# Kernel tuning notes

Hardware: AMD Instinct MI355X
Metric: run time of the kernel (lower is better)

Reference implementation:

```python
import jax, jax.numpy as jnp
import numpy as np

B, S, D, VOCAB = 64, 2048, 256, 288

def setup_inputs() -> dict:
    key = jax.random.key(0)
    k1, k2, k3 = jax.random.split(key, 3)
    TE = jax.random.randint(k1, (B, S, 2), 0, VOCAB, dtype=jnp.int64)
    W1 = jax.random.normal(k2, (VOCAB + 7, D), dtype=jnp.float32) * 0.05
    b1 = jnp.zeros((D,), dtype=jnp.float32)
    W2 = jax.random.normal(k3, (D, D), dtype=jnp.float32) * 0.05
    b2 = jnp.zeros((D,), dtype=jnp.float32)
    return {"TE": TE, "T": VOCAB, "W1": W1, "b1": b1, "W2": W2, "b2": b2}

def reference(TE, T, W1, b1, W2, b2):
    # one_hot(day,7)||one_hot(time,T) @ W1  ==  gather rows of W1 and add
    day = TE[..., 0].astype(jnp.int32) % 7          # [B, S]
    tod = TE[..., 1].astype(jnp.int32) % T          # [B, S]
    h = W1[day] + W1[7 + tod] + b1                  # [B, S, D]  (Linear 1)
    h = jax.nn.relu(h)
    out = jnp.einsum('bsd,de->bse', h, W2) + b2     # [B, S, D]  (Linear 2)
    return out[:, :, None, :]                       # [B, S, 1, D]
```

## Files before the change

kernel.cpp:

```cpp
#include <hip/hip_runtime.h>
#include <hip/hip_bf16.h>


typedef __bf16 bf16x4 __attribute__((ext_vector_type(4)));
typedef __bf16 bf16x8 __attribute__((ext_vector_type(8)));
typedef float  f32x4  __attribute__((ext_vector_type(4)));

#define M_TOTAL   131072
#define BM        128


__global__ __launch_bounds__(64) void prep_all(const float* __restrict__ W1,
                                               const float* __restrict__ b1,
                                               const float* __restrict__ W2,
                                               __bf16* __restrict__ W2S,
                                               __bf16* __restrict__ Htab,
                                               const int* __restrict__ TE32,
                                               int* __restrict__ flag, int T) {
    const int b = blockIdx.x, lane = threadIdx.x;
    const int nTab = 7 * T;
    if (b < nTab) {
        const float* __restrict__ wa = W1 + (b / T) * 256;
        const float* __restrict__ wb = W1 + (7 + b % T) * 256;
        f32x4 a = *(const f32x4*)(wa + lane * 4);
        f32x4 c = *(const f32x4*)(wb + lane * 4);
        f32x4 d = *(const f32x4*)(b1 + lane * 4);
        bf16x4 h;
#pragma unroll
        for (int j = 0; j < 4; ++j) h[j] = (__bf16)fmaxf(a[j] + c[j] + d[j], 0.0f);
        *(bf16x4*)(Htab + b * 256 + lane * 4) = h;
    } else {
        const int wb = b - nTab;
#pragma unroll
        for (int q = 0; q < 2; ++q) {
            int c = (wb * 64 + lane) * 2 + q;
            int l = c & 63, ksnt = c >> 6;
            int ks = ksnt & 7, nt = ksnt >> 3;
            int n  = nt * 16 + (l & 15);
            int k0 = ks * 32 + (l >> 4) * 8;
            bf16x8 w;
#pragma unroll
            for (int j = 0; j < 8; ++j) w[j] = (__bf16)W2[(k0 + j) * 256 + n];
            *(bf16x8*)(W2S + c * 8) = w;
        }
        if (wb == 0) {
            int v = 0;
            for (int i = lane; i < 2048; i += 64) v |= TE32[2 * i + 1];
            unsigned long long nz = __ballot(v != 0);
            if (lane == 0) *flag = (nz == 0ull) ? 1 : 0;
        }
    }
}

__global__ __launch_bounds__(256, 3) void temb_gemm(
        const int*   __restrict__ TE32,
        const __bf16* __restrict__ Htab,
        const __bf16* __restrict__ W2S,
        const float* __restrict__ b2,
        const int*   __restrict__ flag,
        float* __restrict__ out, int T)
{
    __shared__ __bf16 Bs[4 * 8 * 512];

    const int is64 = *flag;
    const int tid  = threadIdx.x;
    const int wave = tid >> 6;
    const int lane = tid & 63;
    const int m    = lane & 15;
    const int quad = lane >> 4;
    const int rowBase = blockIdx.x * BM + wave * 32;

    int code[2];
#pragma unroll
    for (int t = 0; t < 2; ++t) {
        const int row = rowBase + t * 16 + m;
        int day, tod;
        if (is64) { int4 te = *(const int4*)(TE32 + 4 * row); day = te.x; tod = te.z; }
        else      { int2 te = *(const int2*)(TE32 + 2 * row); day = te.x; tod = te.y; }
        code[t] = (day % 7) * T + (tod % T);
    }
    bf16x8 hfrag[2][8];
#pragma unroll
    for (int t = 0; t < 2; ++t)
#pragma unroll
        for (int ks = 0; ks < 8; ++ks)
            hfrag[t][ks] = *(const bf16x8*)(Htab + code[t] * 256 + ks * 32 + quad * 8);

    const bf16x8* __restrict__ gsrc = (const bf16x8*)W2S + tid;
    bf16x8* __restrict__ ldst = (bf16x8*)Bs + tid;
    const bf16x8* __restrict__ lsrc = (const bf16x8*)Bs;

    bf16x8 stage[8];
#pragma unroll
    for (int q = 0; q < 8; ++q) stage[q] = gsrc[q * 256];

    for (int g = 0; g < 4; ++g) {
#pragma unroll
        for (int q = 0; q < 8; ++q) ldst[q * 256] = stage[q];
        __syncthreads();
        if (g < 3) {
#pragma unroll
            for (int q = 0; q < 8; ++q) stage[q] = gsrc[(g + 1) * 2048 + q * 256];
        }
#pragma unroll
        for (int ntl = 0; ntl < 4; ++ntl) {
            const int nt = g * 4 + ntl;
            f32x4 acc0 = {0.f, 0.f, 0.f, 0.f};
            f32x4 acc1 = {0.f, 0.f, 0.f, 0.f};
#pragma unroll
            for (int ks = 0; ks < 8; ++ks) {
                bf16x8 wfrag = lsrc[(ntl * 8 + ks) * 64 + lane];
                acc0 = __builtin_amdgcn_mfma_f32_16x16x32_bf16(wfrag, hfrag[0][ks], acc0, 0, 0, 0);
                acc1 = __builtin_amdgcn_mfma_f32_16x16x32_bf16(wfrag, hfrag[1][ks], acc1, 0, 0, 0);
            }
            const f32x4 bias = *(const f32x4*)(b2 + nt * 16 + quad * 4);
            f32x4 v0, v1;
#pragma unroll
            for (int r = 0; r < 4; ++r) { v0[r] = acc0[r] + bias[r]; v1[r] = acc1[r] + bias[r]; }
            float* p0 = out + (rowBase + m) * 256 + nt * 16 + quad * 4;
            *(f32x4*)p0 = v0;
            *(f32x4*)(p0 + 16 * 256) = v1;
        }
        __syncthreads();
    }
}

extern "C" void kernel_launch(void* const* d_in, const int* in_sizes, int n_in,
                              void* d_out, int out_size, void* d_ws, size_t ws_size,
                              hipStream_t stream) {
    const int*   TE = (const int*)  d_in[0];
    const float* W1 = (const float*)d_in[2];
    const float* b1 = (const float*)d_in[3];
    const float* W2 = (const float*)d_in[4];
    const float* b2 = (const float*)d_in[5];
    const int T = in_sizes[2] / 256 - 7;

    __bf16* W2S  = (__bf16*)d_ws;
    __bf16* Htab = (__bf16*)((char*)d_ws + 131072);
    int*    flag = (int*)((char*)d_ws + 131072 + (size_t)7 * T * 512);
    float*  out  = (float*)d_out;

    prep_all<<<7 * T + 64, 64, 0, stream>>>(W1, b1, W2, W2S, Htab, TE, flag, T);
    temb_gemm<<<M_TOTAL / BM, 256, 0, stream>>>(TE, Htab, W2S, b2, flag, out, T);
}
```

Measured before the change: 166.4 us.

## Precompute full output table per (day,tod) code and gather rows

Because the output depends only on the pair (day, tod), the change computes the full 7*T x 256 output table once with a small MFMA GEMM. The main kernel then becomes a pure gather that copies table rows to the output by code. This removes the per-row GEMM over all 131072 rows and leaves a memory-bound copy bounded by the output write. It needs extra workspace and falls back to the old path if the workspace is too small. It also fixes negative-modulo handling.

```diff
diff --git a/kernel.cpp b/kernel.cpp
--- a/kernel.cpp
+++ b/kernel.cpp
@@ -52,6 +52,108 @@
     }
 }
 
+__global__ __launch_bounds__(256, 3) void otab_gemm(
+        const __bf16* __restrict__ Htab,
+        const __bf16* __restrict__ W2S,
+        const float* __restrict__ b2,
+        float* __restrict__ Otab, int T)
+{
+    __shared__ __bf16 Bs[4 * 8 * 512];
+
+    const int tid  = threadIdx.x;
+    const int wave = tid >> 6;
+    const int lane = tid & 63;
+    const int m    = lane & 15;
+    const int quad = lane >> 4;
+    const int rowBase = blockIdx.x * BM + wave * 32;
+    const int nTab = 7 * T;
+
+    int code[2];
+#pragma unroll
+    for (int t = 0; t < 2; ++t) {
+        int row = rowBase + t * 16 + m;
+        code[t] = row < nTab ? row : nTab - 1;
+    }
+    bf16x8 hfrag[2][8];
+#pragma unroll
+    for (int t = 0; t < 2; ++t)
+#pragma unroll
+        for (int ks = 0; ks < 8; ++ks)
+            hfrag[t][ks] = *(const bf16x8*)(Htab + code[t] * 256 + ks * 32 + quad * 8);
+
+    const bf16x8* __restrict__ gsrc = (const bf16x8*)W2S + tid;
+    bf16x8* __restrict__ ldst = (bf16x8*)Bs + tid;
+    const bf16x8* __restrict__ lsrc = (const bf16x8*)Bs;
+
+    bf16x8 stage[8];
+#pragma unroll
+    for (int q = 0; q < 8; ++q) stage[q] = gsrc[q * 256];
+
+    for (int g = 0; g < 4; ++g) {
+#pragma unroll
+        for (int q = 0; q < 8; ++q) ldst[q * 256] = stage[q];
+        __syncthreads();
+        if (g < 3) {
+#pragma unroll
+            for (int q = 0; q < 8; ++q) stage[q] = gsrc[(g + 1) * 2048 + q * 256];
+        }
+#pragma unroll
+        for (int ntl = 0; ntl < 4; ++ntl) {
+            const int nt = g * 4 + ntl;
+            f32x4 acc0 = {0.f, 0.f, 0.f, 0.f};
+            f32x4 acc1 = {0.f, 0.f, 0.f, 0.f};
+#pragma unroll
+            for (int ks = 0; ks < 8; ++ks) {
+                bf16x8 wfrag = lsrc[(ntl * 8 + ks) * 64 + lane];
+                acc0 = __builtin_amdgcn_mfma_f32_16x16x32_bf16(wfrag, hfrag[0][ks], acc0, 0, 0, 0);
+                acc1 = __builtin_amdgcn_mfma_f32_16x16x32_bf16(wfrag, hfrag[1][ks], acc1, 0, 0, 0);
+            }
+            const f32x4 bias = *(const f32x4*)(b2 + nt * 16 + quad * 4);
+            f32x4 v0, v1;
+#pragma unroll
+            for (int r = 0; r < 4; ++r) { v0[r] = acc0[r] + bias[r]; v1[r] = acc1[r] + bias[r]; }
+            float* p0 = Otab + (rowBase + m) * 256 + nt * 16 + quad * 4;
+            *(f32x4*)p0 = v0;
+            *(f32x4*)(p0 + 16 * 256) = v1;
+        }
+        __syncthreads();
+    }
+}
+
+__global__ __launch_bounds__(256) void gather_out(
+        const int*   __restrict__ TE32,
+        const float* __restrict__ Otab,
+        const int*   __restrict__ flag,
+        float* __restrict__ out, int T)
+{
+    __shared__ int codes[64];
+    const int tid  = threadIdx.x;
+    const int wave = tid >> 6;
+    const int lane = tid & 63;
+    const int rowBase = blockIdx.x * 64;
+
+    if (tid < 64) {
+        const int is64 = *flag;
+        const int row = rowBase + tid;
+        int d32, t32;
+        if (is64) { int4 te = *(const int4*)(TE32 + 4 * row); d32 = te.x; t32 = te.z; }
+        else      { int2 te = *(const int2*)(TE32 + 2 * row); d32 = te.x; t32 = te.y; }
+        int day = d32 % 7; if (day < 0) day += 7;
+        int tod = t32 % T; if (tod < 0) tod += T;
+        codes[tid] = day * T + tod;
+    }
+    __syncthreads();
+
+    const float* src0 = Otab + lane * 4;
+    float*       dst0 = out + (size_t)rowBase * 256 + (size_t)wave * 16 * 256 + lane * 4;
+#pragma unroll
+    for (int r = 0; r < 16; ++r) {
+        const int c = codes[wave * 16 + r];
+        f32x4 v = *(const f32x4*)(src0 + (size_t)c * 256);
+        *(f32x4*)(dst0 + (size_t)r * 256) = v;
+    }
+}
+
 __global__ __launch_bounds__(256, 3) void temb_gemm(
         const int*   __restrict__ TE32,
         const __bf16* __restrict__ Htab,
@@ -77,7 +179,9 @@
         int day, tod;
         if (is64) { int4 te = *(const int4*)(TE32 + 4 * row); day = te.x; tod = te.z; }
         else      { int2 te = *(const int2*)(TE32 + 2 * row); day = te.x; tod = te.y; }
-        code[t] = (day % 7) * T + (tod % T);
+        int dm = day % 7; if (dm < 0) dm += 7;
+        int tm = tod % T; if (tm < 0) tm += T;
+        code[t] = dm * T + tm;
     }
     bf16x8 hfrag[2][8];
 #pragma unroll
@@ -135,11 +239,25 @@
     const float* b2 = (const float*)d_in[5];
     const int T = in_sizes[2] / 256 - 7;
 
+    const int otab_blocks = (7 * T + BM - 1) / BM;
+    const int otab_rows   = otab_blocks * BM;
+
+    const size_t hoff = 131072;
+    const size_t foff = hoff + (size_t)7 * T * 512;
+    const size_t ooff = foff + 256;
+    const size_t need = ooff + (size_t)otab_rows * 1024;
+
     __bf16* W2S  = (__bf16*)d_ws;
-    __bf16* Htab = (__bf16*)((char*)d_ws + 131072);
-    int*    flag = (int*)((char*)d_ws + 131072 + (size_t)7 * T * 512);
+    __bf16* Htab = (__bf16*)((char*)d_ws + hoff);
+    int*    flag = (int*)  ((char*)d_ws + foff);
+    float*  Otab = (float*)((char*)d_ws + ooff);
     float*  out  = (float*)d_out;
 
     prep_all<<<7 * T + 64, 64, 0, stream>>>(W1, b1, W2, W2S, Htab, TE, flag, T);
-    temb_gemm<<<M_TOTAL / BM, 256, 0, stream>>>(TE, Htab, W2S, b2, flag, out, T);
-}
+    if (ws_size >= need) {
+        otab_gemm<<<otab_blocks, 256, 0, stream>>>(Htab, W2S, b2, Otab, T);
+        gather_out<<<M_TOTAL / 64, 256, 0, stream>>>(TE, Otab, flag, out, T);
+    } else {
+        temb_gemm<<<M_TOTAL / BM, 256, 0, stream>>>(TE, Htab, W2S, b2, flag, out, T);
+    }
+}
```

After: 169.6 us. No clear change (+1.9%).
